# Kernel tuning notes

Hardware: AMD Instinct MI355X
Metric: run time of the kernel (lower is better)

The kernel has to match this reference:

```python
import jax, jax.numpy as jnp
import numpy as np

B, H, S, V = 1, 12, 384, 64
D = H * V  # 768, all_head_size
PD_EPS = 1e-6  # torch F.pairwise_distance eps added to the difference


def setup_inputs() -> dict:
    key = jax.random.key(0)
    ks = jax.random.split(key, 8)
    attn = jax.random.uniform(ks[1], (B, H, S, S), dtype=jnp.float32)
    attn = attn / attn.sum(-1, keepdims=True)  # valid probability rows
    return {
        "value_layer": jax.random.normal(ks[0], (B, H, S, V), dtype=jnp.float32),
        "attention_probs": attn,
        "hidden_states": jax.random.normal(ks[2], (B, S, D), dtype=jnp.float32),
        "pre_ln_states": jax.random.normal(ks[3], (B, S, D), dtype=jnp.float32),
        "dense_w": jax.random.normal(ks[4], (D, H, V), dtype=jnp.float32) * 0.02,
        "dense_bias": jax.random.normal(ks[5], (D,), dtype=jnp.float32) * 0.02,
        "ln_weight": jax.random.uniform(ks[6], (D,), dtype=jnp.float32, minval=0.5, maxval=1.5),
        "ln_bias": jax.random.normal(ks[7], (D,), dtype=jnp.float32) * 0.02,
    }


def _l_transform(x, w_ln):
    # x @ (I - ones/d) @ diag(w_ln)  ==  (x - mean(x, -1)) * w_ln
    return (x - jnp.mean(x, axis=-1, keepdims=True)) * w_ln


def reference(value_layer, attention_probs, hidden_states, pre_ln_states,
              dense_w, dense_bias, ln_weight, ln_bias):
    # per-head output projection applied to values: [b,h,s,d]
    transformed = jnp.einsum('bhsv,dhv->bhsd', value_layer, dense_w)
    # attention-weighted, summed over heads (fuses the bhksd intermediate): [b,k,s,d]
    summed = jnp.einsum('bhks,bhsd->bksd', attention_probs, transformed)
    s = hidden_states.shape[1]
    # residual contribution sits on the diagonal s==k: [b,s,k,d]
    residual = jnp.einsum('sk,bsd->bskd', jnp.eye(s, dtype=hidden_states.dtype), hidden_states)
    rwl = summed + residual                        # [b,k,s,d]

    tv = _l_transform(rwl, ln_weight)              # mean-center + gamma scale
    attn_output = tv.sum(axis=2)                   # [b,k,d]
    bias_term = _l_transform(dense_bias, ln_weight)  # [d]

    # torch .std(-1) is unbiased (ddof=1); adding eps before std is a no-op
    std = jnp.std(pre_ln_states, axis=-1, ddof=1)  # [b,s]
    ln_std_coef = (1.0 / std).reshape(1, -1, 1)    # valid since b == 1

    resultant = (attn_output + bias_term) * ln_std_coef + ln_bias   # [b,s,d]
    tv_std = tv * ln_std_coef[..., None]                            # [b,k,s,d]
    tv_norm = jnp.linalg.norm(tv_std, axis=-1)                      # [b,k,s]
    # F.pairwise_distance(x, y, p=1) = || x - y + eps ||_1 over last dim
    importance = -jnp.sum(jnp.abs(tv_std - resultant[:, :, None, :] + PD_EPS), axis=-1)

    return (jnp.squeeze(importance, 0), jnp.squeeze(tv_norm, 0),
            jnp.squeeze(tv_std, 0), jnp.squeeze(resultant, 0))
```

## Files before the change

### kernel.cpp

```cpp
#include <hip/hip_runtime.h>
#include <hip/hip_bf16.h>
#include <math.h>

#define H 12
#define S 384
#define V 64
#define D 768
#define PD_EPS 1e-6f

#define TRANS_N (H*S*D)
#define P_N     (H*S*V)
#define AO_N    (S*D)

#define WS_TRANS 0
#define WS_P     (WS_TRANS + TRANS_N)
#define WS_AO    (WS_P + P_N)
#define WS_MT    (WS_AO + 4*AO_N)
#define WS_COEF  (WS_MT + H*S)
#define WS_MH    (WS_COEF + S)
#define WS_BIAS  (WS_MH + S)

#define OUT_IMP   0
#define OUT_NORM  (S*S)
#define OUT_TVSTD (2*S*S)
#define OUT_RES   (2*S*S + (size_t)S*S*D)

__device__ __forceinline__ float block_sum256(float v, volatile float* tmp){
    #pragma unroll
    for (int m=1;m<64;m<<=1) v += __shfl_xor(v, m, 64);
    int w = threadIdx.x >> 6;
    __syncthreads();
    if ((threadIdx.x & 63)==0) tmp[w] = v;
    __syncthreads();
    return tmp[0]+tmp[1]+tmp[2]+tmp[3];
}

__global__ __launch_bounds__(256) void k_transformed(
    const float* __restrict__ value, const float* __restrict__ dense_w,
    float* __restrict__ ws)
{
    const int h  = blockIdx.x;
    const int s0 = blockIdx.y * 8;
    const int d  = blockIdx.z * 256 + threadIdx.x;
    __shared__ float vals[8*64];
    int t = threadIdx.x;
    vals[t]       = value[(size_t)(h*S + s0 + (t>>6))*V + (t&63)];
    int t2 = t + 256;
    vals[t2]      = value[(size_t)(h*S + s0 + (t2>>6))*V + (t2&63)];
    __syncthreads();
    const float4* wr4 = (const float4*)(dense_w + (size_t)(d*H + h)*V);
    float4 wr[16];
    #pragma unroll
    for (int i=0;i<16;i++) wr[i] = wr4[i];
    float* trans = ws + WS_TRANS;
    #pragma unroll
    for (int si=0; si<8; si++){
        float4 acc = make_float4(0.f,0.f,0.f,0.f);
        const float4* lv4 = (const float4*)(vals + si*64);
        #pragma unroll
        for (int i=0;i<16;i++){
            float4 lv = lv4[i];
            acc.x = fmaf(wr[i].x, lv.x, acc.x);
            acc.y = fmaf(wr[i].y, lv.y, acc.y);
            acc.z = fmaf(wr[i].z, lv.z, acc.z);
            acc.w = fmaf(wr[i].w, lv.w, acc.w);
        }
        trans[(size_t)(h*S + s0 + si)*D + d] = (acc.x+acc.y)+(acc.z+acc.w);
    }
}

__global__ __launch_bounds__(256) void k_prep(
    const float* __restrict__ pre_ln, const float* __restrict__ hidden,
    const float* __restrict__ dense_bias, const float* __restrict__ ln_w,
    float* __restrict__ ws)
{
    __shared__ float tmp[4];
    int b = blockIdx.x;
    int t = threadIdx.x;
    if (b < S){
        float s1=0.f, s2=0.f, hs=0.f;
        #pragma unroll
        for (int j=0;j<3;j++){
            int d = t + j*256;
            float x = pre_ln[(size_t)b*D + d];
            s1 += x; s2 = fmaf(x,x,s2);
            hs += hidden[(size_t)b*D + d];
        }
        float sum1  = block_sum256(s1,tmp);
        float sumsq = block_sum256(s2,tmp);
        float hsum  = block_sum256(hs,tmp);
        if (t==0){
            float var = (sumsq - sum1*sum1/(float)D) / (float)(D-1);
            ws[WS_COEF + b] = 1.0f / sqrtf(var);
            ws[WS_MH + b]   = hsum / (float)D;
        }
    } else if (b == S){
        float s1=0.f;
        #pragma unroll
        for (int j=0;j<3;j++) s1 += dense_bias[t + j*256];
        float mean = block_sum256(s1,tmp) / (float)D;
        #pragma unroll
        for (int j=0;j<3;j++){
            int d = t + j*256;
            ws[WS_BIAS + d] = (dense_bias[d]-mean)*ln_w[d];
        }
    } else {
        int r = b - (S+1);
        float s1=0.f;
        #pragma unroll
        for (int j=0;j<3;j++) s1 += ws[WS_TRANS + (size_t)r*D + t + j*256];
        float sum = block_sum256(s1,tmp);
        if (t==0) ws[WS_MT + r] = sum / (float)D;
    }
}

__global__ __launch_bounds__(256) void k_P(
    const float* __restrict__ attn, const float* __restrict__ value,
    float* __restrict__ ws)
{
    int p = blockIdx.x*4 + (threadIdx.x>>6);
    int lane = threadIdx.x & 63;
    int h = p / S;
    int k = p - h*S;
    const float* ap = attn + (size_t)(h*S + k)*S;
    const float* vp = value + (size_t)h*S*V + lane;
    float a0=0.f,a1=0.f,a2=0.f,a3=0.f;
    for (int s=0;s<S;s+=4){
        a0 = fmaf(ap[s+0], vp[(size_t)(s+0)*V], a0);
        a1 = fmaf(ap[s+1], vp[(size_t)(s+1)*V], a1);
        a2 = fmaf(ap[s+2], vp[(size_t)(s+2)*V], a2);
        a3 = fmaf(ap[s+3], vp[(size_t)(s+3)*V], a3);
    }
    ws[WS_P + (size_t)p*V + lane] = (a0+a1)+(a2+a3);
}

__global__ __launch_bounds__(256) void k_ao(const float* __restrict__ dense_w,
                                            float* __restrict__ ws)
{
    const int d0 = blockIdx.x * 64;
    const int k0 = blockIdx.y * 64;
    const int z  = blockIdx.z;
    __shared__ float As[64][17], Bs[64][17];
    const int tid = threadIdx.x;
    const int tx = tid & 15, ty = tid >> 4;
    float acc[4][4] = {};
    const float* Pw = ws + WS_P;
    for (int c=0;c<12;c++){
        int hv0 = z*192 + c*16;
        #pragma unroll
        for (int e = tid; e < 1024; e += 256){
            int row = e >> 4, col = e & 15;
            int hv = hv0 + col;
            int hh = hv >> 6, vv = hv & 63;
            As[row][col] = Pw[(size_t)(hh*S + k0 + row)*V + vv];
            Bs[row][col] = dense_w[(size_t)(d0 + row)*D + hv];
        }
        __syncthreads();
        #pragma unroll
        for (int kk=0;kk<16;kk++){
            float a[4],bv[4];
            #pragma unroll
            for (int i=0;i<4;i++) a[i]  = As[ty*4+i][kk];
            #pragma unroll
            for (int j=0;j<4;j++) bv[j] = Bs[tx*4+j][kk];
            #pragma unroll
            for (int i=0;i<4;i++)
                #pragma unroll
                for (int j=0;j<4;j++)
                    acc[i][j] = fmaf(a[i], bv[j], acc[i][j]);
        }
        __syncthreads();
    }
    float* ao = ws + WS_AO + (size_t)z*AO_N;
    #pragma unroll
    for (int i=0;i<4;i++)
        #pragma unroll
        for (int j=0;j<4;j++)
            ao[(size_t)(k0+ty*4+i)*D + d0 + tx*4 + j] = acc[i][j];
}

__global__ __launch_bounds__(256) void k_rowfix(
    const float* __restrict__ hidden, const float* __restrict__ ln_w,
    const float* __restrict__ ln_b, float* __restrict__ ws, float* __restrict__ out)
{
    __shared__ float tmp[4];
    int k = blockIdx.x, t = threadIdx.x;
    float sr[3]; float tot = 0.f;
    #pragma unroll
    for (int j=0;j<3;j++){
        int d = t + j*256;
        float v = hidden[(size_t)k*D + d];
        #pragma unroll
        for (int z=0;z<4;z++) v += ws[WS_AO + (size_t)z*AO_N + (size_t)k*D + d];
        sr[j] = v; tot += v;
    }
    float msum = block_sum256(tot,tmp) / (float)D;
    float ck = ws[WS_COEF + k];
    float* res = out + OUT_RES;
    #pragma unroll
    for (int j=0;j<3;j++){
        int d = t + j*256;
        float ao = ln_w[d]*(sr[j]-msum);
        res[(size_t)k*D + d] = (ao + ws[WS_BIAS+d])*ck + ln_b[d];
    }
}

__global__ __launch_bounds__(256) void k_main(
    const float* __restrict__ attn, const float* __restrict__ hidden,
    const float* __restrict__ ln_w, const float* __restrict__ ws,
    float* __restrict__ out)
{
    const int k0 = blockIdx.x * 32;
    const int s  = blockIdx.y;
    const int t  = threadIdx.x;

    __shared__ float att_s[H][32];
    __shared__ float m_s[32];
    __shared__ float c_s[32];
    __shared__ float red[32][8];

    for (int e = t; e < H*32; e += 256){
        int h = e >> 5, kk = e & 31;
        att_s[h][kk] = attn[((size_t)(h*S + k0 + kk))*S + s];
    }

    const float* trans = ws + WS_TRANS;
    float T[H][3];
    #pragma unroll
    for (int h=0;h<H;h++)
        #pragma unroll
        for (int j=0;j<3;j++)
            T[h][j] = trans[(size_t)(h*S + s)*D + t + j*256];
    float wq[3];
    #pragma unroll
    for (int j=0;j<3;j++) wq[j] = ln_w[t + j*256];

    __syncthreads();
    if (t < 32){
        int k = k0 + t;
        float m = 0.f;
        #pragma unroll
        for (int h=0;h<H;h++) m = fmaf(att_s[h][t], ws[WS_MT + h*S + s], m);
        if (k == s) m += ws[WS_MH + k];
        m_s[t] = m;
        c_s[t] = ws[WS_COEF + k];
    }
    __syncthreads();

    const float* res = out + OUT_RES;
    float* tvstd = out + OUT_TVSTD;
    const int lane = t & 63, wv = t >> 6;
    for (int kk=0;kk<32;kk++){
        const int k = k0 + kk;
        float a[H];
        #pragma unroll
        for (int h=0;h<H;h++) a[h] = att_s[h][kk];
        const float m  = m_s[kk];
        const float ck = c_s[kk];
        const bool diag = (k == s);
        float nacc=0.f, iacc=0.f;
        size_t rowbase = ((size_t)k*S + s)*D;
        #pragma unroll
        for (int j=0;j<3;j++){
            int d = t + j*256;
            float r = 0.f;
            #pragma unroll
            for (int h=0;h<H;h++) r = fmaf(a[h], T[h][j], r);
            if (diag) r += hidden[(size_t)k*D + d];
            float tvs = (r - m) * wq[j] * ck;
            __builtin_nontemporal_store(tvs, &tvstd[rowbase + d]);
            nacc = fmaf(tvs,tvs,nacc);
            float diff = tvs - res[(size_t)k*D + d] + PD_EPS;
            iacc += fabsf(diff);
        }
        #pragma unroll
        for (int mm=1;mm<64;mm<<=1){
            nacc += __shfl_xor(nacc, mm, 64);
            iacc += __shfl_xor(iacc, mm, 64);
        }
        if (lane==0){ red[kk][wv] = nacc; red[kk][4+wv] = iacc; }
    }
    __syncthreads();
    if (t < 32){
        int k = k0 + t;
        float n  = red[t][0]+red[t][1]+red[t][2]+red[t][3];
        float ii = red[t][4]+red[t][5]+red[t][6]+red[t][7];
        __builtin_nontemporal_store(sqrtf(n), &out[OUT_NORM + (size_t)k*S + s]);
        __builtin_nontemporal_store(-ii,      &out[OUT_IMP  + (size_t)k*S + s]);
    }
}

extern "C" void kernel_launch(void* const* d_in, const int* in_sizes, int n_in,
                              void* d_out, int out_size, void* d_ws, size_t ws_size,
                              hipStream_t stream)
{
    const float* value   = (const float*)d_in[0];
    const float* attn    = (const float*)d_in[1];
    const float* hidden  = (const float*)d_in[2];
    const float* pre_ln  = (const float*)d_in[3];
    const float* dense_w = (const float*)d_in[4];
    const float* dense_b = (const float*)d_in[5];
    const float* ln_w    = (const float*)d_in[6];
    const float* ln_b    = (const float*)d_in[7];
    float* out = (float*)d_out;
    float* ws  = (float*)d_ws;

    k_transformed<<<dim3(12,48,3),256,0,stream>>>(value, dense_w, ws);
    k_P<<<1152,256,0,stream>>>(attn, value, ws);
    k_prep<<<S+1+H*S,256,0,stream>>>(pre_ln, hidden, dense_b, ln_w, ws);
    k_ao<<<dim3(12,6,4),256,0,stream>>>(dense_w, ws);
    k_rowfix<<<S,256,0,stream>>>(hidden, ln_w, ln_b, ws, out);
    k_main<<<dim3(12,S),256,0,stream>>>(attn, hidden, ln_w, ws, out);
}
```

Before: 608.3 us.

## Use DPP wave reductions, packed LDS rows, and restrict-aliased resultant copy in k_main

Replaces the shfl_xor butterfly reductions in k_main with DPP row-shift/broadcast reductions, whose result is read from lane 63. Attention weights, mean, and coefficient are packed per k into float4 LDS rows so they load as vector reads. The resultant is also written to a workspace copy, so k_main reads it through a restrict pointer instead of from the output buffer it writes. The ln_w*ck product is hoisted out of the inner loop. The hot loop is memory-bound on the large tv_std store, so the compute savings may matter little.

New measurement: 596.2 us. 2.0% less time.

```diff
diff --git a/kernel.cpp b/kernel.cpp
--- a/kernel.cpp
+++ b/kernel.cpp
@@ -33,6 +33,21 @@
     if ((threadIdx.x & 63)==0) tmp[w] = v;
     __syncthreads();
     return tmp[0]+tmp[1]+tmp[2]+tmp[3];
+}
+
+template<int CTRL, int RMASK>
+__device__ __forceinline__ float dppadd(float x){
+    int y = __builtin_amdgcn_update_dpp(0, __float_as_int(x), CTRL, RMASK, 0xf, true);
+    return x + __int_as_float(y);
+}
+__device__ __forceinline__ float wave_sum64(float x){
+    x = dppadd<0x111, 0xf>(x);
+    x = dppadd<0x112, 0xf>(x);
+    x = dppadd<0x114, 0xf>(x);
+    x = dppadd<0x118, 0xf>(x);
+    x = dppadd<0x142, 0xa>(x);
+    x = dppadd<0x143, 0xc>(x);
+    return x;
 }
 
 __global__ __launch_bounds__(256) void k_transformed(
@@ -201,7 +216,9 @@
     for (int j=0;j<3;j++){
         int d = t + j*256;
         float ao = ln_w[d]*(sr[j]-msum);
-        res[(size_t)k*D + d] = (ao + ws[WS_BIAS+d])*ck + ln_b[d];
+        float val = (ao + ws[WS_BIAS+d])*ck + ln_b[d];
+        res[(size_t)k*D + d] = val;
+        ws[WS_P + (size_t)k*D + d] = val;
     }
 }
 
@@ -214,14 +231,13 @@
     const int s  = blockIdx.y;
     const int t  = threadIdx.x;
 
-    __shared__ float att_s[H][32];
-    __shared__ float m_s[32];
-    __shared__ float c_s[32];
-    __shared__ float red[32][8];
+    __shared__ float4 row4[32][4];
+    __shared__ float2 red2[32][4];
+    float* rowf = (float*)row4;
 
     for (int e = t; e < H*32; e += 256){
         int h = e >> 5, kk = e & 31;
-        att_s[h][kk] = attn[((size_t)(h*S + k0 + kk))*S + s];
+        rowf[kk*16 + h] = attn[((size_t)(h*S + k0 + kk))*S + s];
     }
 
     const float* trans = ws + WS_TRANS;
@@ -240,51 +256,57 @@
         int k = k0 + t;
         float m = 0.f;
         #pragma unroll
-        for (int h=0;h<H;h++) m = fmaf(att_s[h][t], ws[WS_MT + h*S + s], m);
+        for (int h=0;h<H;h++) m = fmaf(rowf[t*16 + h], ws[WS_MT + h*S + s], m);
         if (k == s) m += ws[WS_MH + k];
-        m_s[t] = m;
-        c_s[t] = ws[WS_COEF + k];
-    }
-    __syncthreads();
-
-    const float* res = out + OUT_RES;
+        rowf[t*16 + 12] = m;
+        rowf[t*16 + 13] = ws[WS_COEF + k];
+    }
+    __syncthreads();
+
+    const float* __restrict__ resw = ws + WS_P;
     float* tvstd = out + OUT_TVSTD;
     const int lane = t & 63, wv = t >> 6;
     for (int kk=0;kk<32;kk++){
         const int k = k0 + kk;
-        float a[H];
-        #pragma unroll
-        for (int h=0;h<H;h++) a[h] = att_s[h][kk];
-        const float m  = m_s[kk];
-        const float ck = c_s[kk];
+        float4 A0 = row4[kk][0], A1 = row4[kk][1], A2 = row4[kk][2], A3 = row4[kk][3];
+        const float m = A3.x, ck = A3.y;
         const bool diag = (k == s);
+        const float wc[3] = {wq[0]*ck, wq[1]*ck, wq[2]*ck};
         float nacc=0.f, iacc=0.f;
         size_t rowbase = ((size_t)k*S + s)*D;
+        const float* resr = resw + (size_t)k*D;
         #pragma unroll
         for (int j=0;j<3;j++){
             int d = t + j*256;
-            float r = 0.f;
-            #pragma unroll
-            for (int h=0;h<H;h++) r = fmaf(a[h], T[h][j], r);
+            float r;
+            r = A0.x * T[0][j];
+            r = fmaf(A0.y, T[1][j],  r);
+            r = fmaf(A0.z, T[2][j],  r);
+            r = fmaf(A0.w, T[3][j],  r);
+            r = fmaf(A1.x, T[4][j],  r);
+            r = fmaf(A1.y, T[5][j],  r);
+            r = fmaf(A1.z, T[6][j],  r);
+            r = fmaf(A1.w, T[7][j],  r);
+            r = fmaf(A2.x, T[8][j],  r);
+            r = fmaf(A2.y, T[9][j],  r);
+            r = fmaf(A2.z, T[10][j], r);
+            r = fmaf(A2.w, T[11][j], r);
             if (diag) r += hidden[(size_t)k*D + d];
-            float tvs = (r - m) * wq[j] * ck;
+            float tvs = (r - m) * wc[j];
             __builtin_nontemporal_store(tvs, &tvstd[rowbase + d]);
             nacc = fmaf(tvs,tvs,nacc);
-            float diff = tvs - res[(size_t)k*D + d] + PD_EPS;
-            iacc += fabsf(diff);
-        }
-        #pragma unroll
-        for (int mm=1;mm<64;mm<<=1){
-            nacc += __shfl_xor(nacc, mm, 64);
-            iacc += __shfl_xor(iacc, mm, 64);
-        }
-        if (lane==0){ red[kk][wv] = nacc; red[kk][4+wv] = iacc; }
+            iacc += fabsf(tvs - resr[d] + PD_EPS);
+        }
+        nacc = wave_sum64(nacc);
+        iacc = wave_sum64(iacc);
+        if (lane==63) red2[kk][wv] = make_float2(nacc, iacc);
     }
     __syncthreads();
     if (t < 32){
         int k = k0 + t;
-        float n  = red[t][0]+red[t][1]+red[t][2]+red[t][3];
-        float ii = red[t][4]+red[t][5]+red[t][6]+red[t][7];
+        float2 q0=red2[t][0], q1=red2[t][1], q2=red2[t][2], q3=red2[t][3];
+        float n  = q0.x+q1.x+q2.x+q3.x;
+        float ii = q0.y+q1.y+q2.y+q3.y;
         __builtin_nontemporal_store(sqrtf(n), &out[OUT_NORM + (size_t)k*S + s]);
         __builtin_nontemporal_store(-ii,      &out[OUT_IMP  + (size_t)k*S + s]);
     }
```
